# Optimization experiments

Hardware: AMD Instinct MI355X
Metric: run time of the kernel (lower is better)

The kernel has to match this reference:

```python
import jax, jax.numpy as jnp
import numpy as np

S, B, H = 2048, 32, 1024

def setup_inputs() -> dict:
    key = jax.random.key(0)
    ks = jax.random.split(key, 5)
    hidden = jax.random.normal(ks[0], (B, H), dtype=jnp.float32)
    encoder_outputs = jax.random.normal(ks[1], (S, B, H), dtype=jnp.float32)
    source_lengths = jax.random.randint(ks[2], (B,), 1, S + 1, dtype=jnp.int32)
    attn_w = jax.random.normal(ks[3], (H, 2 * H), dtype=jnp.float32) / np.sqrt(2 * H)
    attn_b = jnp.zeros((H,), dtype=jnp.float32)
    v = jax.random.uniform(ks[4], (H,), dtype=jnp.float32)
    return {"hidden": hidden, "encoder_outputs": encoder_outputs,
            "source_lengths": source_lengths, "attn_w": attn_w,
            "attn_b": attn_b, "v": v}

def reference(hidden, encoder_outputs, source_lengths, attn_w, attn_b, v):
    s, b, h = encoder_outputs.shape
    # Broadcast decoder hidden over source positions: (S,B,H)
    hid = jnp.broadcast_to(hidden[None, :, :], (s, b, h))
    cat = jnp.concatenate([hid, encoder_outputs], axis=2)          # (S,B,2H)
    energy = jnp.tanh(jnp.einsum('sbk,hk->sbh', cat, attn_w) + attn_b)  # (S,B,H)
    scores = jnp.einsum('sbh,h->bs', energy, v)                     # (B,S)
    mask = jnp.arange(s)[None, :] < source_lengths[:, None]         # (B,S)
    scores = jnp.where(mask, scores, jnp.float32(-1e10))
    attention_weights = jax.nn.softmax(scores, axis=1)              # (B,S)
    context = jnp.einsum('bs,sbh->bh', attention_weights, encoder_outputs)
    return context, attention_weights
```

## Files before the change

kernel.cpp:

```cpp
#include <hip/hip_runtime.h>

#define S_DIM 2048
#define B_DIM 32
#define H_DIM 1024
#define ROWS  (S_DIM * B_DIM)

typedef __attribute__((ext_vector_type(4))) float    f32x4;
typedef __attribute__((ext_vector_type(8))) _Float16 f16x8;
typedef __attribute__((ext_vector_type(2))) __fp16   h16x2;

__device__ __forceinline__ unsigned short f16_bits(float f) {
  union { _Float16 h; unsigned short u; } cv;
  cv.h = (_Float16)f;
  return cv.u;
}

__device__ __forceinline__ float fast_tanh(float x) {
  x = fminf(15.0f, fmaxf(-15.0f, x));
  float z = __expf(-2.0f * x);
  return (1.0f - z) * __builtin_amdgcn_rcpf(1.0f + z);
}

__device__ __forceinline__ void load_lds16(const void* g, void* l) {
  __builtin_amdgcn_global_load_lds(
      (const __attribute__((address_space(1))) unsigned int*)g,
      (__attribute__((address_space(3))) unsigned int*)l, 16, 0, 0);
}

__global__ void prep_kernel(const float* __restrict__ hidden,
                            const float* __restrict__ attn_w,
                            const float* __restrict__ attn_b,
                            float* __restrict__ hp,
                            unsigned short* __restrict__ Bp,
                            float* __restrict__ scores,
                            float* __restrict__ ctx) {
  int bid = blockIdx.x, tid = threadIdx.x;
  if (bid < 64) {
    int hl = tid >> 4;
    int kp = tid & 15;
    int h  = bid * 16 + hl;
    const f32x4* wrow = (const f32x4*)(attn_w + (size_t)h * (2 * H_DIM)) + kp * 16;
    f32x4 w[16];
#pragma unroll
    for (int j = 0; j < 16; ++j) w[j] = wrow[j];
    float bias = attn_b[h];
    for (int b = 0; b < B_DIM; ++b) {
      const f32x4* xrow = (const f32x4*)(hidden + (size_t)b * H_DIM) + kp * 16;
      float s = 0.f;
#pragma unroll
      for (int j = 0; j < 16; ++j) {
        f32x4 x = xrow[j];
        s = fmaf(w[j].x, x.x, s); s = fmaf(w[j].y, x.y, s);
        s = fmaf(w[j].z, x.z, s); s = fmaf(w[j].w, x.w, s);
      }
      s += __shfl_xor(s, 1); s += __shfl_xor(s, 2);
      s += __shfl_xor(s, 4); s += __shfl_xor(s, 8);
      if (kp == 0) hp[(size_t)b * H_DIM + h] = s + bias;
    }
  } else if (bid < 576) {
    int id = (bid - 64) * 256 + tid;
    int slot = id & 7;
    int n    = (id >> 3) & 127;
    int step = (id >> 10) & 15;
    int g    = id >> 14;
    int sub  = slot ^ (n & 7);
    int h    = g * 128 + n;
    const float* src = attn_w + (size_t)h * (2 * H_DIM) + H_DIM + step * 64 + sub * 8;
    f32x4 a = *(const f32x4*)src;
    f32x4 b = *(const f32x4*)(src + 4);
    ushort4 lo, hi;
    lo.x = f16_bits(a.x); lo.y = f16_bits(a.y); lo.z = f16_bits(a.z); lo.w = f16_bits(a.w);
    hi.x = f16_bits(b.x); hi.y = f16_bits(b.y); hi.z = f16_bits(b.z); hi.w = f16_bits(b.w);
    *(ushort4*)(Bp + (size_t)id * 8)     = lo;
    *(ushort4*)(Bp + (size_t)id * 8 + 4) = hi;
  } else if (bid < 640) {
    int idx = (bid - 576) * 256 + tid;
    *(f32x4*)(scores + (size_t)idx * 4) = (f32x4){0.f, 0.f, 0.f, 0.f};
  } else {
    int idx = (bid - 640) * 256 + tid;
    *(f32x4*)(ctx + (size_t)idx * 4) = (f32x4){0.f, 0.f, 0.f, 0.f};
  }
}

__global__ __launch_bounds__(256, 4)
void gemm_scores_kernel(const float* __restrict__ enc,
                        const unsigned short* __restrict__ Bp,
                        const float* __restrict__ hp,
                        const float* __restrict__ v,
                        float* __restrict__ scores) {
  __shared__ __align__(16) unsigned short As[1024 * 8];
  __shared__ __align__(16) unsigned short Bs[1024 * 8];
  const int tid  = threadIdx.x;
  const int lane = tid & 63;
  const int wid  = tid >> 6;
  const int wm   = wid >> 1;
  const int wn   = wid & 1;
  const int m16  = lane & 15;
  const int quad = lane >> 4;
  const int rx   = m16 & 7;
  const int bid  = blockIdx.x;
  const int xcd  = bid & 7;
  const int slot = bid >> 3;
  const int t    = xcd * 64 + (slot >> 3);
  const int g    = slot & 7;

  f32x4 acc[4][4];
#pragma unroll
  for (int i = 0; i < 4; ++i)
#pragma unroll
    for (int j = 0; j < 4; ++j) acc[i][j] = (f32x4){0.f, 0.f, 0.f, 0.f};

  const float* aBase = enc + (size_t)t * 128 * H_DIM;
  const unsigned short* bBase = Bp + (size_t)g * 16 * 8192;

  int aR[4], aSub[4];
#pragma unroll
  for (int c = 0; c < 4; ++c) {
    int q = c * 256 + tid;
    aR[c] = q >> 3;
    aSub[c] = (q & 7) ^ (aR[c] & 7);
  }

  for (int step = 0; step < 16; ++step) {
    const unsigned short* bS = bBase + (size_t)step * 8192;
#pragma unroll
    for (int c = 0; c < 4; ++c) {
      int q = c * 256 + tid;
      load_lds16(bS + (size_t)q * 8, Bs + q * 8);
    }
#pragma unroll
    for (int c = 0; c < 4; ++c) {
      int q = c * 256 + tid;
      const float* s = aBase + (size_t)aR[c] * H_DIM + step * 64 + aSub[c] * 8;
      f32x4 a = *(const f32x4*)s;
      f32x4 b = *(const f32x4*)(s + 4);
      union { f16x8 v8; h16x2 h2[4]; } pk;
      pk.h2[0] = __builtin_amdgcn_cvt_pkrtz(a.x, a.y);
      pk.h2[1] = __builtin_amdgcn_cvt_pkrtz(a.z, a.w);
      pk.h2[2] = __builtin_amdgcn_cvt_pkrtz(b.x, b.y);
      pk.h2[3] = __builtin_amdgcn_cvt_pkrtz(b.z, b.w);
      *(f16x8*)(As + q * 8) = pk.v8;
    }
    __syncthreads();

#pragma unroll
    for (int ko = 0; ko < 2; ++ko) {
      int sl = (ko * 4 + quad) ^ rx;
      f16x8 af[4], bfr[4];
#pragma unroll
      for (int f = 0; f < 4; ++f) {
        int r = wm * 64 + f * 16 + m16;
        af[f] = *(const f16x8*)&As[r * 64 + sl * 8];
      }
#pragma unroll
      for (int f = 0; f < 4; ++f) {
        int n = wn * 64 + f * 16 + m16;
        bfr[f] = *(const f16x8*)&Bs[n * 64 + sl * 8];
      }
#pragma unroll
      for (int mf = 0; mf < 4; ++mf)
#pragma unroll
        for (int nf = 0; nf < 4; ++nf)
          acc[mf][nf] = __builtin_amdgcn_mfma_f32_16x16x32_f16(
              af[mf], bfr[nf], acc[mf][nf], 0, 0, 0);
    }
    __syncthreads();
  }

  const int row0 = t * 128, n0 = g * 128;
#pragma unroll
  for (int mf = 0; mf < 4; ++mf) {
#pragma unroll
    for (int reg = 0; reg < 4; ++reg) {
      int row_g = row0 + wm * 64 + mf * 16 + quad * 4 + reg;
      int b     = row_g & 31;
      int s     = row_g >> 5;
      float psum = 0.f;
#pragma unroll
      for (int nf = 0; nf < 4; ++nf) {
        int col = n0 + wn * 64 + nf * 16 + m16;
        float e = acc[mf][nf][reg] + hp[b * H_DIM + col];
        e = fast_tanh(e);
        psum = fmaf(e, v[col], psum);
      }
      psum += __shfl_xor(psum, 1);
      psum += __shfl_xor(psum, 2);
      psum += __shfl_xor(psum, 4);
      psum += __shfl_xor(psum, 8);
      if (m16 == 0) atomicAdd(&scores[b * S_DIM + s], psum);
    }
  }
}

__global__ void softmax_kernel(const float* __restrict__ scores,
                               const int* __restrict__ lens,
                               float* __restrict__ wout) {
  int b = blockIdx.x, tid = threadIdx.x;
  int len = lens[b];
  float vals[8];
  float m = -3.0e38f;
#pragma unroll
  for (int i = 0; i < 8; ++i) {
    int s = i * 256 + tid;
    float x = scores[b * S_DIM + s];
    vals[i] = (s < len) ? x : -3.0e38f;
    m = fmaxf(m, vals[i]);
  }
#pragma unroll
  for (int off = 32; off > 0; off >>= 1) m = fmaxf(m, __shfl_xor(m, off));
  __shared__ float redm[4], reds[4];
  int wid = tid >> 6, lane = tid & 63;
  if (lane == 0) redm[wid] = m;
  __syncthreads();
  m = fmaxf(fmaxf(redm[0], redm[1]), fmaxf(redm[2], redm[3]));

  float e[8];
  float sum = 0.f;
#pragma unroll
  for (int i = 0; i < 8; ++i) {
    int s = i * 256 + tid;
    e[i] = (s < len) ? __expf(vals[i] - m) : 0.f;
    sum += e[i];
  }
#pragma unroll
  for (int off = 32; off > 0; off >>= 1) sum += __shfl_xor(sum, off);
  if (lane == 0) reds[wid] = sum;
  __syncthreads();
  sum = reds[0] + reds[1] + reds[2] + reds[3];
  float inv = 1.0f / sum;
#pragma unroll
  for (int i = 0; i < 8; ++i)
    wout[b * S_DIM + i * 256 + tid] = e[i] * inv;
}

__global__ void context_kernel(const float* __restrict__ enc,
                               const float* __restrict__ wts,
                               const int* __restrict__ lens,
                               float* __restrict__ ctx) {
  int sc = blockIdx.x;
  int b  = blockIdx.y;
  int len = lens[b];
  int s0 = sc * 128;
  if (s0 >= len) return;
  int cnt = min(128, len - s0);
  int tid = threadIdx.x;
  f32x4 acc = (f32x4){0.f, 0.f, 0.f, 0.f};
  const float* wrow = wts + (size_t)b * S_DIM + s0;
#pragma unroll 4
  for (int i = 0; i < cnt; ++i) {
    float w = wrow[i];
    f32x4 e = *(const f32x4*)(enc + ((size_t)(s0 + i) * B_DIM + b) * H_DIM + tid * 4);
    acc.x = fmaf(w, e.x, acc.x);
    acc.y = fmaf(w, e.y, acc.y);
    acc.z = fmaf(w, e.z, acc.z);
    acc.w = fmaf(w, e.w, acc.w);
  }
  float* dst = ctx + (size_t)b * H_DIM + tid * 4;
  atomicAdd(dst + 0, acc.x);
  atomicAdd(dst + 1, acc.y);
  atomicAdd(dst + 2, acc.z);
  atomicAdd(dst + 3, acc.w);
}

extern "C" void kernel_launch(void* const* d_in, const int* in_sizes, int n_in,
                              void* d_out, int out_size, void* d_ws, size_t ws_size,
                              hipStream_t stream) {
  const float* hidden = (const float*)d_in[0];
  const float* enc    = (const float*)d_in[1];
  const int*   lens   = (const int*)d_in[2];
  const float* attn_w = (const float*)d_in[3];
  const float* attn_b = (const float*)d_in[4];
  const float* v      = (const float*)d_in[5];

  float* out_ctx = (float*)d_out;
  float* out_w   = (float*)d_out + B_DIM * H_DIM;

  char* p = (char*)d_ws;
  float* scores = (float*)p;               p += (size_t)B_DIM * S_DIM * 4;
  float* hp     = (float*)p;               p += (size_t)B_DIM * H_DIM * 4;
  unsigned short* Bp = (unsigned short*)p;

  hipLaunchKernelGGL(prep_kernel, dim3(672), dim3(256), 0, stream,
                     hidden, attn_w, attn_b, hp, Bp, scores, out_ctx);
  hipLaunchKernelGGL(gemm_scores_kernel, dim3(4096), dim3(256), 0, stream,
                     enc, Bp, hp, v, scores);
  hipLaunchKernelGGL(softmax_kernel, dim3(B_DIM), dim3(256), 0, stream,
                     scores, lens, out_w);
  hipLaunchKernelGGL(context_kernel, dim3(16, B_DIM), dim3(256), 0, stream,
                     enc, out_w, lens, out_ctx);
}
```

Before: 604.8 us.

## Load A fragments directly from global into registers and double-buffer B in LDS

The GEMM kernel no longer stages the fp32 encoder tile through LDS. Each wave loads its A fragments straight from global memory into registers and converts them to fp16 just before the MFMAs. The B tile becomes double-buffered in LDS, so the next step's async loads overlap the current compute and one barrier per step is dropped. In exchange, the two waves that share rows (wn=0/1) now each read the same A data from global, and register pressure rises, so launch bounds drop to 3 blocks per CU.

```diff
diff --git a/kernel.cpp b/kernel.cpp
--- a/kernel.cpp
+++ b/kernel.cpp
@@ -82,14 +82,13 @@
   }
 }
 
-__global__ __launch_bounds__(256, 4)
+__global__ __launch_bounds__(256, 3)
 void gemm_scores_kernel(const float* __restrict__ enc,
                         const unsigned short* __restrict__ Bp,
                         const float* __restrict__ hp,
                         const float* __restrict__ v,
                         float* __restrict__ scores) {
-  __shared__ __align__(16) unsigned short As[1024 * 8];
-  __shared__ __align__(16) unsigned short Bs[1024 * 8];
+  __shared__ __align__(16) unsigned short Bs[2][1024 * 8];
   const int tid  = threadIdx.x;
   const int lane = tid & 63;
   const int wid  = tid >> 6;
@@ -113,58 +112,63 @@
   const float* aBase = enc + (size_t)t * 128 * H_DIM;
   const unsigned short* bBase = Bp + (size_t)g * 16 * 8192;
 
-  int aR[4], aSub[4];
-#pragma unroll
-  for (int c = 0; c < 4; ++c) {
-    int q = c * 256 + tid;
-    aR[c] = q >> 3;
-    aSub[c] = (q & 7) ^ (aR[c] & 7);
-  }
-
-  for (int step = 0; step < 16; ++step) {
-    const unsigned short* bS = bBase + (size_t)step * 8192;
+  size_t aOff[4];
+#pragma unroll
+  for (int f = 0; f < 4; ++f)
+    aOff[f] = (size_t)(wm * 64 + f * 16 + m16) * H_DIM + quad * 8;
+
+  {
+    const unsigned short* bS = bBase;
 #pragma unroll
     for (int c = 0; c < 4; ++c) {
       int q = c * 256 + tid;
-      load_lds16(bS + (size_t)q * 8, Bs + q * 8);
-    }
-#pragma unroll
-    for (int c = 0; c < 4; ++c) {
-      int q = c * 256 + tid;
-      const float* s = aBase + (size_t)aR[c] * H_DIM + step * 64 + aSub[c] * 8;
-      f32x4 a = *(const f32x4*)s;
-      f32x4 b = *(const f32x4*)(s + 4);
-      union { f16x8 v8; h16x2 h2[4]; } pk;
-      pk.h2[0] = __builtin_amdgcn_cvt_pkrtz(a.x, a.y);
-      pk.h2[1] = __builtin_amdgcn_cvt_pkrtz(a.z, a.w);
-      pk.h2[2] = __builtin_amdgcn_cvt_pkrtz(b.x, b.y);
-      pk.h2[3] = __builtin_amdgcn_cvt_pkrtz(b.z, b.w);
-      *(f16x8*)(As + q * 8) = pk.v8;
-    }
+      load_lds16(bS + (size_t)q * 8, &Bs[0][q * 8]);
+    }
+  }
+
+  for (int step = 0; step < 16; ++step) {
     __syncthreads();
+    if (step < 15) {
+      const unsigned short* bS = bBase + (size_t)(step + 1) * 8192;
+      unsigned short* dstb = &Bs[(step + 1) & 1][0];
+#pragma unroll
+      for (int c = 0; c < 4; ++c) {
+        int q = c * 256 + tid;
+        load_lds16(bS + (size_t)q * 8, dstb + q * 8);
+      }
+    }
+    const unsigned short* bsb = &Bs[step & 1][0];
+    const float* aStep = aBase + step * 64;
 
 #pragma unroll
     for (int ko = 0; ko < 2; ++ko) {
+      f32x4 a0[4], a1[4];
+#pragma unroll
+      for (int f = 0; f < 4; ++f) {
+        const float* ap = aStep + aOff[f] + ko * 32;
+        a0[f] = *(const f32x4*)ap;
+        a1[f] = *(const f32x4*)(ap + 4);
+      }
       int sl = (ko * 4 + quad) ^ rx;
-      f16x8 af[4], bfr[4];
-#pragma unroll
-      for (int f = 0; f < 4; ++f) {
-        int r = wm * 64 + f * 16 + m16;
-        af[f] = *(const f16x8*)&As[r * 64 + sl * 8];
-      }
+      f16x8 bfr[4];
 #pragma unroll
       for (int f = 0; f < 4; ++f) {
         int n = wn * 64 + f * 16 + m16;
-        bfr[f] = *(const f16x8*)&Bs[n * 64 + sl * 8];
-      }
-#pragma unroll
-      for (int mf = 0; mf < 4; ++mf)
+        bfr[f] = *(const f16x8*)&bsb[n * 64 + sl * 8];
+      }
+#pragma unroll
+      for (int mf = 0; mf < 4; ++mf) {
+        union { f16x8 v8; h16x2 h2[4]; } pk;
+        pk.h2[0] = __builtin_amdgcn_cvt_pkrtz(a0[mf].x, a0[mf].y);
+        pk.h2[1] = __builtin_amdgcn_cvt_pkrtz(a0[mf].z, a0[mf].w);
+        pk.h2[2] = __builtin_amdgcn_cvt_pkrtz(a1[mf].x, a1[mf].y);
+        pk.h2[3] = __builtin_amdgcn_cvt_pkrtz(a1[mf].z, a1[mf].w);
 #pragma unroll
         for (int nf = 0; nf < 4; ++nf)
           acc[mf][nf] = __builtin_amdgcn_mfma_f32_16x16x32_f16(
-              af[mf], bfr[nf], acc[mf][nf], 0, 0, 0);
-    }
-    __syncthreads();
+              pk.v8, bfr[nf], acc[mf][nf], 0, 0, 0);
+      }
+    }
   }
 
   const int row0 = t * 128, n0 = g * 128;
```

New measurement: 913.6 us. 51.1% more time.
